# Kernel tuning notes

Measured on AMD Instinct MI355X. Metric: run time of the kernel, lower is better.

## Reference

```python
import jax, jax.numpy as jnp
import numpy as np

N = 4096      # num_nodes
E = 16384     # edges per layer view
PHI = 64      # phi_dim
BETA = 0.5
EPS = 1e-8
LM = 1.0      # len(policy) per layer


def _mlp(x, w1, b1, w2, b2):
    # x: [E,1]; Linear(1,PHI) -> ReLU -> Linear(PHI,1)
    h = jax.nn.relu(x * w1[None, :] + b1[None, :])   # [E,PHI]
    return h @ w2[:, None] + b2                      # [E,1]


def setup_inputs() -> dict:
    key = jax.random.key(0)
    ks = jax.random.split(key, 16)
    inp = {
        "A": jax.random.uniform(ks[0], (N, N), dtype=jnp.float32),
        "src0": jax.random.randint(ks[1], (E,), 0, N),
        "dst0": jax.random.randint(ks[2], (E,), 0, N),
        "src1": jax.random.randint(ks[3], (E,), 0, N),
        "dst1": jax.random.randint(ks[4], (E,), 0, N),
        "f0": jax.random.normal(ks[5], (N, 1), dtype=jnp.float32),
        "f1": jax.random.normal(ks[6], (N, 1), dtype=jnp.float32),
        "phi1_w1": jax.random.normal(ks[7], (2, PHI), dtype=jnp.float32) * 0.5,
        "phi1_b1": jax.random.normal(ks[8], (2, PHI), dtype=jnp.float32) * 0.1,
        "phi1_w2": jax.random.normal(ks[9], (2, PHI), dtype=jnp.float32) * 0.5,
        "phi1_b2": jax.random.normal(ks[10], (2,), dtype=jnp.float32) * 0.1,
        "phi2_w1": jax.random.normal(ks[11], (2, PHI), dtype=jnp.float32) * 0.5,
        "phi2_b1": jax.random.normal(ks[12], (2, PHI), dtype=jnp.float32) * 0.1,
        "phi2_w2": jax.random.normal(ks[13], (2, PHI), dtype=jnp.float32) * 0.5,
        "phi2_b2": jax.random.normal(ks[14], (2,), dtype=jnp.float32) * 0.1,
    }
    return inp


def reference(A, src0, dst0, src1, dst1, f0, f1,
              phi1_w1, phi1_b1, phi1_w2, phi1_b2,
              phi2_w1, phi2_b1, phi2_w2, phi2_b2):
    # mean node struct feature across the two merged layer views: [N]
    f_mean = (0.5 * (f0 + f1))[:, 0]
    outs = []
    for lid, (src, dst) in enumerate([(src0, dst0), (src1, dst1)]):
        # gathered, feature-weighted adjacency rows: [E, N]
        mat_src = A[src] * f_mean[None, :]
        mat_dst = A[dst] * f_mean[None, :]
        # diag(mat_src @ mat_dst.T) == per-edge dot product: [E]
        out_struct = jnp.sum(mat_src * mat_dst, axis=-1)
        # random_fill with f_dropout=0 -> deterministic +eps, then row norms
        d_src = jnp.linalg.norm(mat_src + EPS, axis=-1)
        d_dst = jnp.linalg.norm(mat_dst + EPS, axis=-1)
        out_n = (out_struct / (d_src * d_dst))[:, None]      # [E,1]
        y1 = _mlp(out_n, phi1_w1[lid], phi1_b1[lid], phi1_w2[lid], phi1_b2[lid])
        sl1 = BETA * (y1 / LM)
        outs.append(_mlp(sl1, phi2_w1[lid], phi2_b1[lid], phi2_w2[lid], phi2_b2[lid]))
    return tuple(outs)
```

## Files before the change

### kernel.cpp

```cpp
#include <hip/hip_runtime.h>

#define N_NODES 4096
#define EDGES   16384
#define PHI     64
#define EPS_F   1e-8f
#define BETA_F  0.5f
#define NCHUNK  8
#define WCHUNK  512

__device__ __forceinline__ float wave_sum(float v) {
#pragma unroll
    for (int off = 32; off > 0; off >>= 1) v += __shfl_xor(v, off, 64);
    return v;
}

__device__ __forceinline__ unsigned int pack_bf16(float f) {
    unsigned int u = __float_as_uint(f);
    u += 0x7fffu + ((u >> 16) & 1u);
    return u >> 16;
}

__global__ void k_prep(const float* __restrict__ f0, const float* __restrict__ f1,
                       float* __restrict__ fm, float* __restrict__ wsq) {
    int i = blockIdx.x * blockDim.x + threadIdx.x;
    if (i < N_NODES) {
        float m = 0.5f * (f0[i] + f1[i]);
        fm[i]  = m;
        wsq[i] = m * m;
    }
}

__global__ void __launch_bounds__(256) k_rows_fast(const float* __restrict__ A,
                                                   const float* __restrict__ f0,
                                                   const float* __restrict__ f1,
                                                   unsigned short* __restrict__ B,
                                                   float* __restrict__ dnorm) {
    int row = blockIdx.x;
    const float4* a4  = (const float4*)(A + (size_t)row * N_NODES);
    const float4* f04 = (const float4*)f0;
    const float4* f14 = (const float4*)f1;
    uint2* b2 = (uint2*)(B + (size_t)row * N_NODES);
    int t = threadIdx.x;
    float acc = 0.f;
#pragma unroll
    for (int i = 0; i < 4; ++i) {
        int idx = i * 256 + t;
        float4 a = a4[idx];
        float4 fa = f04[idx];
        float4 fb = f14[idx];
        float fx = 0.5f * (fa.x + fb.x), fy = 0.5f * (fa.y + fb.y);
        float fz = 0.5f * (fa.z + fb.z), fw = 0.5f * (fa.w + fb.w);
        float b0 = a.x * fx, b1 = a.y * fy, b2v = a.z * fz, b3 = a.w * fw;
        float e0 = b0 + EPS_F, e1 = b1 + EPS_F, e2 = b2v + EPS_F, e3 = b3 + EPS_F;
        acc += e0 * e0 + e1 * e1 + e2 * e2 + e3 * e3;
        uint2 p;
        p.x = (pack_bf16(b1) << 16) | pack_bf16(b0);
        p.y = (pack_bf16(b3) << 16) | pack_bf16(b2v);
        b2[idx] = p;
    }
    acc = wave_sum(acc);
    __shared__ float red[4];
    if ((t & 63) == 0) red[t >> 6] = acc;
    __syncthreads();
    if (t == 0) dnorm[row] = sqrtf(red[0] + red[1] + red[2] + red[3]);
}

__global__ void __launch_bounds__(256) k_rows_slow(const float* __restrict__ A,
                                                   const float* __restrict__ fm,
                                                   float* __restrict__ dnorm) {
    int row = blockIdx.x;
    const float4* a4  = (const float4*)(A + (size_t)row * N_NODES);
    const float4* fm4 = (const float4*)fm;
    int t = threadIdx.x;
    float acc = 0.f;
#pragma unroll
    for (int i = 0; i < 4; ++i) {
        int idx = i * 256 + t;
        float4 a = a4[idx];
        float4 f = fm4[idx];
        float e0 = a.x * f.x + EPS_F, e1 = a.y * f.y + EPS_F;
        float e2 = a.z * f.z + EPS_F, e3 = a.w * f.w + EPS_F;
        acc += e0 * e0 + e1 * e1 + e2 * e2 + e3 * e3;
    }
    acc = wave_sum(acc);
    __shared__ float red[4];
    if ((t & 63) == 0) red[t >> 6] = acc;
    __syncthreads();
    if (t == 0) dnorm[row] = sqrtf(red[0] + red[1] + red[2] + red[3]);
}

__device__ __forceinline__ void mlp_epilogue(float x, int lid, int e, int lane,
                                             const float* __restrict__ p1w1, const float* __restrict__ p1b1,
                                             const float* __restrict__ p1w2, const float* __restrict__ p1b2,
                                             const float* __restrict__ p2w1, const float* __restrict__ p2b1,
                                             const float* __restrict__ p2w2, const float* __restrict__ p2b2,
                                             float* __restrict__ out) {
    int wi = lid * PHI + lane;
    float h1 = fmaxf(fmaf(x, p1w1[wi], p1b1[wi]), 0.f);
    float y1 = wave_sum(h1 * p1w2[wi]) + p1b2[lid];
    float sl1 = BETA_F * y1;
    float h2 = fmaxf(fmaf(sl1, p2w1[wi], p2b1[wi]), 0.f);
    float y2 = wave_sum(h2 * p2w2[wi]) + p2b2[lid];
    if (lane == 0) out[lid * EDGES + e] = y2;
}

__global__ void __launch_bounds__(256, 8) k_edges_chunk(
        const unsigned short* __restrict__ B,
        const int* __restrict__ src0, const int* __restrict__ dst0,
        const int* __restrict__ src1, const int* __restrict__ dst1,
        float* __restrict__ P) {
    int blk   = blockIdx.x;
    int chunk = blk & (NCHUNK - 1);
    int slot  = blk >> 3;
    int wave  = threadIdx.x >> 6;
    int lane  = threadIdx.x & 63;
    int g     = lane >> 3;
    int sub   = lane & 7;

    int ge  = slot * 32 + wave * 8 + g;
    int lid = ge >> 14;
    int e   = ge & (EDGES - 1);
    int s = lid ? src1[e] : src0[e];
    int d = lid ? dst1[e] : dst0[e];

    const uint4* rs = (const uint4*)(B + (size_t)s * N_NODES + chunk * WCHUNK) + sub;
    const uint4* rd = (const uint4*)(B + (size_t)d * N_NODES + chunk * WCHUNK) + sub;

    float acc = 0.f;
#pragma unroll
    for (int h = 0; h < 2; ++h) {
        uint4 us[4], ud[4];
#pragma unroll
        for (int i = 0; i < 4; ++i) {
            us[i] = rs[(h * 4 + i) * 8];
            ud[i] = rd[(h * 4 + i) * 8];
        }
#pragma unroll
        for (int i = 0; i < 4; ++i) {
#define ACC_U(U, V)                                                    \
            {                                                          \
                float sl = __uint_as_float((U) << 16);                 \
                float sh = __uint_as_float((U) & 0xffff0000u);         \
                float dl = __uint_as_float((V) << 16);                 \
                float dh = __uint_as_float((V) & 0xffff0000u);         \
                acc = fmaf(sl, dl, acc);                               \
                acc = fmaf(sh, dh, acc);                               \
            }
            ACC_U(us[i].x, ud[i].x); ACC_U(us[i].y, ud[i].y);
            ACC_U(us[i].z, ud[i].z); ACC_U(us[i].w, ud[i].w);
#undef ACC_U
        }
    }
    acc += __shfl_xor(acc, 1, 64);
    acc += __shfl_xor(acc, 2, 64);
    acc += __shfl_xor(acc, 4, 64);
    if (sub == 0) P[(size_t)chunk * (2 * EDGES) + ge] = acc;
}

__global__ void __launch_bounds__(256) k_finish(
        const float* __restrict__ P, const float* __restrict__ dnorm,
        const int* __restrict__ src0, const int* __restrict__ dst0,
        const int* __restrict__ src1, const int* __restrict__ dst1,
        const float* __restrict__ p1w1, const float* __restrict__ p1b1,
        const float* __restrict__ p1w2, const float* __restrict__ p1b2,
        const float* __restrict__ p2w1, const float* __restrict__ p2b1,
        const float* __restrict__ p2w2, const float* __restrict__ p2b2,
        float* __restrict__ out) {
    int gw   = (int)((blockIdx.x * blockDim.x + threadIdx.x) >> 6);
    int lane = threadIdx.x & 63;
    int lid  = gw >> 14;
    int e    = gw & (EDGES - 1);
    int s = lid ? src1[e] : src0[e];
    int d = lid ? dst1[e] : dst0[e];
    float acc = 0.f;
#pragma unroll
    for (int c = 0; c < NCHUNK; ++c) acc += P[(size_t)c * (2 * EDGES) + gw];
    float x = acc / (dnorm[s] * dnorm[d]);
    mlp_epilogue(x, lid, e, lane, p1w1, p1b1, p1w2, p1b2, p2w1, p2b1, p2w2, p2b2, out);
}

__global__ void __launch_bounds__(256) k_edges_fast(
        const unsigned short* __restrict__ B, const float* __restrict__ dnorm,
        const int* __restrict__ src0, const int* __restrict__ dst0,
        const int* __restrict__ src1, const int* __restrict__ dst1,
        const float* __restrict__ p1w1, const float* __restrict__ p1b1,
        const float* __restrict__ p1w2, const float* __restrict__ p1b2,
        const float* __restrict__ p2w1, const float* __restrict__ p2b1,
        const float* __restrict__ p2w2, const float* __restrict__ p2b2,
        float* __restrict__ out) {
    int gw   = (int)((blockIdx.x * blockDim.x + threadIdx.x) >> 6);
    int lane = threadIdx.x & 63;
    int lid  = gw >> 14;
    int e    = gw & (EDGES - 1);
    int s = lid ? src1[e] : src0[e];
    int d = lid ? dst1[e] : dst0[e];
    const uint4* rs = (const uint4*)(B + (size_t)s * N_NODES);
    const uint4* rd = (const uint4*)(B + (size_t)d * N_NODES);
    float acc = 0.f;
#pragma unroll
    for (int i = 0; i < 8; ++i) {
        uint4 us = rs[i * 64 + lane];
        uint4 ud = rd[i * 64 + lane];
#define ACC_U(U, V)                                                    \
        {                                                              \
            float sl = __uint_as_float((U) << 16);                     \
            float sh = __uint_as_float((U) & 0xffff0000u);             \
            float dl = __uint_as_float((V) << 16);                     \
            float dh = __uint_as_float((V) & 0xffff0000u);             \
            acc = fmaf(sl, dl, acc);                                   \
            acc = fmaf(sh, dh, acc);                                   \
        }
        ACC_U(us.x, ud.x); ACC_U(us.y, ud.y); ACC_U(us.z, ud.z); ACC_U(us.w, ud.w);
#undef ACC_U
    }
    acc = wave_sum(acc);
    float x = acc / (dnorm[s] * dnorm[d]);
    mlp_epilogue(x, lid, e, lane, p1w1, p1b1, p1w2, p1b2, p2w1, p2b1, p2w2, p2b2, out);
}

__global__ void __launch_bounds__(256) k_edges_slow(
        const float* __restrict__ A, const float* __restrict__ wsq,
        const float* __restrict__ dnorm,
        const int* __restrict__ src0, const int* __restrict__ dst0,
        const int* __restrict__ src1, const int* __restrict__ dst1,
        const float* __restrict__ p1w1, const float* __restrict__ p1b1,
        const float* __restrict__ p1w2, const float* __restrict__ p1b2,
        const float* __restrict__ p2w1, const float* __restrict__ p2b1,
        const float* __restrict__ p2w2, const float* __restrict__ p2b2,
        float* __restrict__ out) {
    __shared__ float wl[N_NODES];
    int t = threadIdx.x;
    const float4* w4 = (const float4*)wsq;
    float4* wl4 = (float4*)wl;
    for (int i = t; i < N_NODES / 4; i += 256) wl4[i] = w4[i];
    __syncthreads();

    int gw   = (int)((blockIdx.x * blockDim.x + t) >> 6);
    int lane = t & 63;
    int lid  = gw >> 14;
    int e    = gw & (EDGES - 1);
    int s = lid ? src1[e] : src0[e];
    int d = lid ? dst1[e] : dst0[e];
    const float4* rs = (const float4*)(A + (size_t)s * N_NODES);
    const float4* rd = (const float4*)(A + (size_t)d * N_NODES);
    float acc = 0.f;
#pragma unroll
    for (int i = 0; i < 16; ++i) {
        int idx = i * 64 + lane;
        float4 a = rs[idx];
        float4 b = rd[idx];
        float4 w = wl4[idx];
        acc = fmaf(a.x * b.x, w.x, acc);
        acc = fmaf(a.y * b.y, w.y, acc);
        acc = fmaf(a.z * b.z, w.z, acc);
        acc = fmaf(a.w * b.w, w.w, acc);
    }
    acc = wave_sum(acc);
    float x = acc / (dnorm[s] * dnorm[d]);
    mlp_epilogue(x, lid, e, lane, p1w1, p1b1, p1w2, p1b2, p2w1, p2b1, p2w2, p2b2, out);
}

extern "C" void kernel_launch(void* const* d_in, const int* in_sizes, int n_in,
                              void* d_out, int out_size, void* d_ws, size_t ws_size,
                              hipStream_t stream) {
    const float* A    = (const float*)d_in[0];
    const int*   src0 = (const int*)d_in[1];
    const int*   dst0 = (const int*)d_in[2];
    const int*   src1 = (const int*)d_in[3];
    const int*   dst1 = (const int*)d_in[4];
    const float* f0   = (const float*)d_in[5];
    const float* f1   = (const float*)d_in[6];
    const float* p1w1 = (const float*)d_in[7];
    const float* p1b1 = (const float*)d_in[8];
    const float* p1w2 = (const float*)d_in[9];
    const float* p1b2 = (const float*)d_in[10];
    const float* p2w1 = (const float*)d_in[11];
    const float* p2b1 = (const float*)d_in[12];
    const float* p2w2 = (const float*)d_in[13];
    const float* p2b2 = (const float*)d_in[14];
    float* out = (float*)d_out;

    float* ws  = (float*)d_ws;
    float* fm  = ws;
    float* wsq = ws + N_NODES;
    float* dn  = ws + 2 * N_NODES;
    float* P   = ws + 3 * N_NODES;
    unsigned short* Bnew = (unsigned short*)(P + NCHUNK * 2 * EDGES);
    unsigned short* Bold = (unsigned short*)(ws + 3 * N_NODES);

    size_t need_new = (3ull * N_NODES + (size_t)NCHUNK * 2 * EDGES) * 4
                      + (size_t)N_NODES * N_NODES * 2;
    size_t need_old = 3ull * N_NODES * 4 + (size_t)N_NODES * N_NODES * 2;

    if (ws_size >= need_new) {
        k_rows_fast<<<N_NODES, 256, 0, stream>>>(A, f0, f1, Bnew, dn);
        k_edges_chunk<<<(2 * EDGES * NCHUNK) / 32, 256, 0, stream>>>(
            Bnew, src0, dst0, src1, dst1, P);
        k_finish<<<(2 * EDGES * 64) / 256, 256, 0, stream>>>(
            P, dn, src0, dst0, src1, dst1,
            p1w1, p1b1, p1w2, p1b2, p2w1, p2b1, p2w2, p2b2, out);
    } else if (ws_size >= need_old) {
        k_prep<<<N_NODES / 256, 256, 0, stream>>>(f0, f1, fm, wsq);
        k_rows_fast<<<N_NODES, 256, 0, stream>>>(A, f0, f1, Bold, dn);
        k_edges_fast<<<(2 * EDGES * 64) / 256, 256, 0, stream>>>(
            Bold, dn, src0, dst0, src1, dst1,
            p1w1, p1b1, p1w2, p1b2, p2w1, p2b1, p2w2, p2b2, out);
    } else {
        k_prep<<<N_NODES / 256, 256, 0, stream>>>(f0, f1, fm, wsq);
        k_rows_slow<<<N_NODES, 256, 0, stream>>>(A, fm, dn);
        k_edges_slow<<<(2 * EDGES * 64) / 256, 256, 0, stream>>>(
            A, wsq, dn, src0, dst0, src1, dst1,
            p1w1, p1b1, p1w2, p1b2, p2w1, p2b1, p2w2, p2b2, out);
    }
}
```

Measured before the change: 156.7 us.

## Quantize weighted adjacency rows to int8 and use sdot4 for edge dot products

Replaces the bf16 staging of the feature-weighted adjacency rows with symmetric int8 quantization. A global max-abs scale is computed from the mean features, and the edge kernel accumulates with integer dot4 (sdot4) instead of unpacking bf16 to float FMAs. This halves the bytes gathered per edge row and the staging buffer size, and the chunk count drops from 8 to 4 to match the larger per-chunk byte width. The cost is much coarser precision: since A is in [0,1), quantization error may be significant for small products, risking correctness tolerance.

```diff
diff --git a/kernel.cpp b/kernel.cpp
--- a/kernel.cpp
+++ b/kernel.cpp
@@ -5,8 +5,22 @@
 #define PHI     64
 #define EPS_F   1e-8f
 #define BETA_F  0.5f
-#define NCHUNK  8
-#define WCHUNK  512
+#define NCHUNK  4
+#define WCHUNK  1024
+
+#if __has_builtin(__builtin_amdgcn_sdot4)
+__device__ __forceinline__ int dot4(int a, int b, int c) {
+    return __builtin_amdgcn_sdot4(a, b, c, false);
+}
+#else
+__device__ __forceinline__ int dot4(int a, int b, int c) {
+    c += ((a << 24) >> 24) * ((b << 24) >> 24);
+    c += ((a << 16) >> 24) * ((b << 16) >> 24);
+    c += ((a << 8)  >> 24) * ((b << 8)  >> 24);
+    c += (a >> 24) * (b >> 24);
+    return c;
+}
+#endif
 
 __device__ __forceinline__ float wave_sum(float v) {
 #pragma unroll
@@ -19,6 +33,161 @@
     u += 0x7fffu + ((u >> 16) & 1u);
     return u >> 16;
 }
+
+
+__global__ void __launch_bounds__(1024) k_prep_q(const float* __restrict__ f0,
+                                                 const float* __restrict__ f1,
+                                                 float* __restrict__ fm,
+                                                 float* __restrict__ fmq,
+                                                 float* __restrict__ sc) {
+    int t = threadIdx.x;
+    float4 a = ((const float4*)f0)[t];
+    float4 b = ((const float4*)f1)[t];
+    float4 m;
+    m.x = 0.5f * (a.x + b.x); m.y = 0.5f * (a.y + b.y);
+    m.z = 0.5f * (a.z + b.z); m.w = 0.5f * (a.w + b.w);
+    ((float4*)fm)[t] = m;
+    float mx = fmaxf(fmaxf(fabsf(m.x), fabsf(m.y)), fmaxf(fabsf(m.z), fabsf(m.w)));
+#pragma unroll
+    for (int off = 32; off > 0; off >>= 1) mx = fmaxf(mx, __shfl_xor(mx, off, 64));
+    __shared__ float red[16];
+    __shared__ float s_scale;
+    int lane = t & 63, wid = t >> 6;
+    if (lane == 0) red[wid] = mx;
+    __syncthreads();
+    if (t == 0) {
+        float s = red[0];
+#pragma unroll
+        for (int i = 1; i < 16; ++i) s = fmaxf(s, red[i]);
+        s = fmaxf(s, 1e-20f);
+        s_scale = 127.f / s;
+        sc[0] = 127.f / s;
+        sc[1] = (s / 127.f) * (s / 127.f);
+    }
+    __syncthreads();
+    float q = s_scale;
+    float4 mq;
+    mq.x = m.x * q; mq.y = m.y * q; mq.z = m.z * q; mq.w = m.w * q;
+    ((float4*)fmq)[t] = mq;
+}
+
+__global__ void __launch_bounds__(256) k_rows_q(const float* __restrict__ A,
+                                                const float* __restrict__ fm,
+                                                const float* __restrict__ fmq,
+                                                int* __restrict__ Bq,
+                                                float* __restrict__ dnorm) {
+    int row = blockIdx.x;
+    const float4* a4 = (const float4*)(A + (size_t)row * N_NODES);
+    const float4* m4 = (const float4*)fm;
+    const float4* q4 = (const float4*)fmq;
+    int* brow = Bq + (size_t)row * (N_NODES / 4);
+    int t = threadIdx.x;
+    float acc = 0.f;
+#pragma unroll
+    for (int i = 0; i < 4; ++i) {
+        int idx = i * 256 + t;
+        float4 a = a4[idx];
+        float4 m = m4[idx];
+        float4 mq = q4[idx];
+        float b0 = a.x * m.x, b1 = a.y * m.y, b2 = a.z * m.z, b3 = a.w * m.w;
+        float e0 = b0 + EPS_F, e1 = b1 + EPS_F, e2 = b2 + EPS_F, e3 = b3 + EPS_F;
+        acc += e0 * e0 + e1 * e1 + e2 * e2 + e3 * e3;
+        int q0 = __float2int_rn(a.x * mq.x) & 255;
+        int q1 = __float2int_rn(a.y * mq.y) & 255;
+        int q2 = __float2int_rn(a.z * mq.z) & 255;
+        int q3 = __float2int_rn(a.w * mq.w);
+        brow[idx] = q0 | (q1 << 8) | (q2 << 16) | (q3 << 24);
+    }
+    acc = wave_sum(acc);
+    __shared__ float red[4];
+    if ((t & 63) == 0) red[t >> 6] = acc;
+    __syncthreads();
+    if (t == 0) dnorm[row] = sqrtf(red[0] + red[1] + red[2] + red[3]);
+}
+
+__global__ void __launch_bounds__(256, 8) k_edges_i8(
+        const char* __restrict__ B,
+        const int* __restrict__ src0, const int* __restrict__ dst0,
+        const int* __restrict__ src1, const int* __restrict__ dst1,
+        int* __restrict__ P) {
+    int blk   = blockIdx.x;
+    int chunk = blk & (NCHUNK - 1);
+    int slot  = blk >> 2;
+    int wave  = threadIdx.x >> 6;
+    int lane  = threadIdx.x & 63;
+    int g     = lane >> 3;
+    int sub   = lane & 7;
+
+    int ge  = slot * 32 + wave * 8 + g;
+    int lid = ge >> 14;
+    int e   = ge & (EDGES - 1);
+    int s = lid ? src1[e] : src0[e];
+    int d = lid ? dst1[e] : dst0[e];
+
+    const int4* rs = (const int4*)(B + (size_t)s * N_NODES + chunk * WCHUNK) + sub;
+    const int4* rd = (const int4*)(B + (size_t)d * N_NODES + chunk * WCHUNK) + sub;
+
+    int acc = 0;
+#pragma unroll
+    for (int h = 0; h < 2; ++h) {
+        int4 us[4], ud[4];
+#pragma unroll
+        for (int i = 0; i < 4; ++i) {
+            us[i] = rs[(h * 4 + i) * 8];
+            ud[i] = rd[(h * 4 + i) * 8];
+        }
+#pragma unroll
+        for (int i = 0; i < 4; ++i) {
+            acc = dot4(us[i].x, ud[i].x, acc);
+            acc = dot4(us[i].y, ud[i].y, acc);
+            acc = dot4(us[i].z, ud[i].z, acc);
+            acc = dot4(us[i].w, ud[i].w, acc);
+        }
+    }
+    acc += __shfl_xor(acc, 1, 64);
+    acc += __shfl_xor(acc, 2, 64);
+    acc += __shfl_xor(acc, 4, 64);
+    if (sub == 0) P[(size_t)chunk * (2 * EDGES) + ge] = acc;
+}
+
+__device__ __forceinline__ void mlp_epilogue(float x, int lid, int e, int lane,
+                                             const float* __restrict__ p1w1, const float* __restrict__ p1b1,
+                                             const float* __restrict__ p1w2, const float* __restrict__ p1b2,
+                                             const float* __restrict__ p2w1, const float* __restrict__ p2b1,
+                                             const float* __restrict__ p2w2, const float* __restrict__ p2b2,
+                                             float* __restrict__ out) {
+    int wi = lid * PHI + lane;
+    float h1 = fmaxf(fmaf(x, p1w1[wi], p1b1[wi]), 0.f);
+    float y1 = wave_sum(h1 * p1w2[wi]) + p1b2[lid];
+    float sl1 = BETA_F * y1;
+    float h2 = fmaxf(fmaf(sl1, p2w1[wi], p2b1[wi]), 0.f);
+    float y2 = wave_sum(h2 * p2w2[wi]) + p2b2[lid];
+    if (lane == 0) out[lid * EDGES + e] = y2;
+}
+
+__global__ void __launch_bounds__(256) k_finish_i8(
+        const int* __restrict__ P, const float* __restrict__ dnorm,
+        const float* __restrict__ sc,
+        const int* __restrict__ src0, const int* __restrict__ dst0,
+        const int* __restrict__ src1, const int* __restrict__ dst1,
+        const float* __restrict__ p1w1, const float* __restrict__ p1b1,
+        const float* __restrict__ p1w2, const float* __restrict__ p1b2,
+        const float* __restrict__ p2w1, const float* __restrict__ p2b1,
+        const float* __restrict__ p2w2, const float* __restrict__ p2b2,
+        float* __restrict__ out) {
+    int gw   = (int)((blockIdx.x * blockDim.x + threadIdx.x) >> 6);
+    int lane = threadIdx.x & 63;
+    int lid  = gw >> 14;
+    int e    = gw & (EDGES - 1);
+    int s = lid ? src1[e] : src0[e];
+    int d = lid ? dst1[e] : dst0[e];
+    int acc = 0;
+#pragma unroll
+    for (int c = 0; c < NCHUNK; ++c) acc += P[(size_t)c * (2 * EDGES) + gw];
+    float x = (float)acc * sc[1] / (dnorm[s] * dnorm[d]);
+    mlp_epilogue(x, lid, e, lane, p1w1, p1b1, p1w2, p1b2, p2w1, p2b1, p2w2, p2b2, out);
+}
+
 
 __global__ void k_prep(const float* __restrict__ f0, const float* __restrict__ f1,
                        float* __restrict__ fm, float* __restrict__ wsq) {
@@ -87,96 +256,6 @@
     if ((t & 63) == 0) red[t >> 6] = acc;
     __syncthreads();
     if (t == 0) dnorm[row] = sqrtf(red[0] + red[1] + red[2] + red[3]);
-}
-
-__device__ __forceinline__ void mlp_epilogue(float x, int lid, int e, int lane,
-                                             const float* __restrict__ p1w1, const float* __restrict__ p1b1,
-                                             const float* __restrict__ p1w2, const float* __restrict__ p1b2,
-                                             const float* __restrict__ p2w1, const float* __restrict__ p2b1,
-                                             const float* __restrict__ p2w2, const float* __restrict__ p2b2,
-                                             float* __restrict__ out) {
-    int wi = lid * PHI + lane;
-    float h1 = fmaxf(fmaf(x, p1w1[wi], p1b1[wi]), 0.f);
-    float y1 = wave_sum(h1 * p1w2[wi]) + p1b2[lid];
-    float sl1 = BETA_F * y1;
-    float h2 = fmaxf(fmaf(sl1, p2w1[wi], p2b1[wi]), 0.f);
-    float y2 = wave_sum(h2 * p2w2[wi]) + p2b2[lid];
-    if (lane == 0) out[lid * EDGES + e] = y2;
-}
-
-__global__ void __launch_bounds__(256, 8) k_edges_chunk(
-        const unsigned short* __restrict__ B,
-        const int* __restrict__ src0, const int* __restrict__ dst0,
-        const int* __restrict__ src1, const int* __restrict__ dst1,
-        float* __restrict__ P) {
-    int blk   = blockIdx.x;
-    int chunk = blk & (NCHUNK - 1);
-    int slot  = blk >> 3;
-    int wave  = threadIdx.x >> 6;
-    int lane  = threadIdx.x & 63;
-    int g     = lane >> 3;
-    int sub   = lane & 7;
-
-    int ge  = slot * 32 + wave * 8 + g;
-    int lid = ge >> 14;
-    int e   = ge & (EDGES - 1);
-    int s = lid ? src1[e] : src0[e];
-    int d = lid ? dst1[e] : dst0[e];
-
-    const uint4* rs = (const uint4*)(B + (size_t)s * N_NODES + chunk * WCHUNK) + sub;
-    const uint4* rd = (const uint4*)(B + (size_t)d * N_NODES + chunk * WCHUNK) + sub;
-
-    float acc = 0.f;
-#pragma unroll
-    for (int h = 0; h < 2; ++h) {
-        uint4 us[4], ud[4];
-#pragma unroll
-        for (int i = 0; i < 4; ++i) {
-            us[i] = rs[(h * 4 + i) * 8];
-            ud[i] = rd[(h * 4 + i) * 8];
-        }
-#pragma unroll
-        for (int i = 0; i < 4; ++i) {
-#define ACC_U(U, V)                                                    \
-            {                                                          \
-                float sl = __uint_as_float((U) << 16);                 \
-                float sh = __uint_as_float((U) & 0xffff0000u);         \
-                float dl = __uint_as_float((V) << 16);                 \
-                float dh = __uint_as_float((V) & 0xffff0000u);         \
-                acc = fmaf(sl, dl, acc);                               \
-                acc = fmaf(sh, dh, acc);                               \
-            }
-            ACC_U(us[i].x, ud[i].x); ACC_U(us[i].y, ud[i].y);
-            ACC_U(us[i].z, ud[i].z); ACC_U(us[i].w, ud[i].w);
-#undef ACC_U
-        }
-    }
-    acc += __shfl_xor(acc, 1, 64);
-    acc += __shfl_xor(acc, 2, 64);
-    acc += __shfl_xor(acc, 4, 64);
-    if (sub == 0) P[(size_t)chunk * (2 * EDGES) + ge] = acc;
-}
-
-__global__ void __launch_bounds__(256) k_finish(
-        const float* __restrict__ P, const float* __restrict__ dnorm,
-        const int* __restrict__ src0, const int* __restrict__ dst0,
-        const int* __restrict__ src1, const int* __restrict__ dst1,
-        const float* __restrict__ p1w1, const float* __restrict__ p1b1,
-        const float* __restrict__ p1w2, const float* __restrict__ p1b2,
-        const float* __restrict__ p2w1, const float* __restrict__ p2b1,
-        const float* __restrict__ p2w2, const float* __restrict__ p2b2,
-        float* __restrict__ out) {
-    int gw   = (int)((blockIdx.x * blockDim.x + threadIdx.x) >> 6);
-    int lane = threadIdx.x & 63;
-    int lid  = gw >> 14;
-    int e    = gw & (EDGES - 1);
-    int s = lid ? src1[e] : src0[e];
-    int d = lid ? dst1[e] : dst0[e];
-    float acc = 0.f;
-#pragma unroll
-    for (int c = 0; c < NCHUNK; ++c) acc += P[(size_t)c * (2 * EDGES) + gw];
-    float x = acc / (dnorm[s] * dnorm[d]);
-    mlp_epilogue(x, lid, e, lane, p1w1, p1b1, p1w2, p1b2, p2w1, p2b1, p2w2, p2b2, out);
 }
 
 __global__ void __launch_bounds__(256) k_edges_fast(
@@ -280,27 +359,29 @@
     const float* p2b2 = (const float*)d_in[14];
     float* out = (float*)d_out;
 
-    float* ws  = (float*)d_ws;
-    float* fm  = ws;
-    float* wsq = ws + N_NODES;
-    float* dn  = ws + 2 * N_NODES;
-    float* P   = ws + 3 * N_NODES;
-    unsigned short* Bnew = (unsigned short*)(P + NCHUNK * 2 * EDGES);
+    float* ws = (float*)d_ws;
+    float* fm   = ws;
+    float* fmq  = ws + 4096;
+    float* dn   = ws + 8192;
+    float* sc   = ws + 12288;
+    int*   P    = (int*)(ws + 12352);
+    int*   Bq   = (int*)(ws + 12352 + NCHUNK * 2 * EDGES);
+    size_t need_i8 = (12352ull + (size_t)NCHUNK * 2 * EDGES) * 4
+                     + (size_t)N_NODES * N_NODES;
+
+    float* wsq  = ws + N_NODES;
     unsigned short* Bold = (unsigned short*)(ws + 3 * N_NODES);
-
-    size_t need_new = (3ull * N_NODES + (size_t)NCHUNK * 2 * EDGES) * 4
-                      + (size_t)N_NODES * N_NODES * 2;
     size_t need_old = 3ull * N_NODES * 4 + (size_t)N_NODES * N_NODES * 2;
 
-    if (ws_size >= need_new) {
-        k_rows_fast<<<N_NODES, 256, 0, stream>>>(A, f0, f1, Bnew, dn);
-        k_edges_chunk<<<(2 * EDGES * NCHUNK) / 32, 256, 0, stream>>>(
-            Bnew, src0, dst0, src1, dst1, P);
-        k_finish<<<(2 * EDGES * 64) / 256, 256, 0, stream>>>(
-            P, dn, src0, dst0, src1, dst1,
+    if (ws_size >= need_i8) {
+        k_prep_q<<<1, 1024, 0, stream>>>(f0, f1, fm, fmq, sc);
+        k_rows_q<<<N_NODES, 256, 0, stream>>>(A, fm, fmq, Bq, dn);
+        k_edges_i8<<<(2 * EDGES * NCHUNK) / 32, 256, 0, stream>>>(
+            (const char*)Bq, src0, dst0, src1, dst1, P);
+        k_finish_i8<<<(2 * EDGES * 64) / 256, 256, 0, stream>>>(
+            P, dn, sc, src0, dst0, src1, dst1,
             p1w1, p1b1, p1w2, p1b2, p2w1, p2b1, p2w2, p2b2, out);
     } else if (ws_size >= need_old) {
-        k_prep<<<N_NODES / 256, 256, 0, stream>>>(f0, f1, fm, wsq);
         k_rows_fast<<<N_NODES, 256, 0, stream>>>(A, f0, f1, Bold, dn);
         k_edges_fast<<<(2 * EDGES * 64) / 256, 256, 0, stream>>>(
             Bold, dn, src0, dst0, src1, dst1,
```

After: 145.7 us. -7.0%, faster.
